# Kernel optimization log

Measured on AMD Instinct MI355X. Metric: run time of the kernel, lower is better.

## Reference

```python
import jax, jax.numpy as jnp
import numpy as np
import math

GROUPS = 16
EPS = 1e-5

def setup_inputs() -> dict:
    key = jax.random.key(0)
    ks = jax.random.split(key, 6)
    c = 256
    x = jax.random.normal(ks[0], (4, c, 64, 64), dtype=jnp.float32)
    gn_w = jnp.ones((c,), dtype=jnp.float32)
    gn_b = jnp.zeros((c,), dtype=jnp.float32)
    qkv_w = jax.random.normal(ks[1], (3 * c, c), dtype=jnp.float32) * (1.0 / math.sqrt(c))
    qkv_b = jax.random.normal(ks[2], (3 * c,), dtype=jnp.float32) * 0.02
    proj_w = jax.random.normal(ks[3], (c, c), dtype=jnp.float32) * (1.0 / math.sqrt(c))
    proj_b = jax.random.normal(ks[4], (c,), dtype=jnp.float32) * 0.02
    return {"x": x, "gn_w": gn_w, "gn_b": gn_b, "qkv_w": qkv_w,
            "qkv_b": qkv_b, "proj_w": proj_w, "proj_b": proj_b}

def group_norm(x, w, b):
    bsz, c, h, wd = x.shape
    xg = x.reshape(bsz, GROUPS, c // GROUPS, h, wd)
    mu = xg.mean(axis=(2, 3, 4), keepdims=True)
    var = xg.var(axis=(2, 3, 4), keepdims=True)
    xn = ((xg - mu) * jax.lax.rsqrt(var + EPS)).reshape(bsz, c, h, wd)
    return xn * w[None, :, None, None] + b[None, :, None, None]

def reference(x, gn_w, gn_b, qkv_w, qkv_b, proj_w, proj_b):
    b, c, h, w = x.shape
    xn = group_norm(x, gn_w, gn_b)
    # 1x1 conv == channel matmul: [b,3c,h,w]
    qkv = jnp.einsum('oc,bchw->bohw', qkv_w, xn) + qkv_b[None, :, None, None]
    q, k, v = jnp.split(qkv, 3, axis=1)          # each [b,c,h,w]
    n = h * w
    q = q.reshape(b, c, n).transpose(0, 2, 1)    # [b,n,c]
    k = k.reshape(b, c, n)                       # [b,c,n]
    v = v.reshape(b, c, n).transpose(0, 2, 1)    # [b,n,c]
    scores = jnp.einsum('bqc,bck->bqk', q, k) / jnp.sqrt(jnp.float32(c))
    attn = jax.nn.softmax(scores, axis=-1)       # [b,n,n]
    out = jnp.einsum('bqk,bkc->bqc', attn, v)    # [b,n,c]
    out = out.transpose(0, 2, 1).reshape(b, c, h, w)
    out = jnp.einsum('oc,bchw->bohw', proj_w, out) + proj_b[None, :, None, None]
    return x + out
```

## Files before the change

### kernel.cpp

```cpp
#include <hip/hip_runtime.h>


typedef unsigned short u16;
typedef unsigned char  u8;
typedef __attribute__((ext_vector_type(8)))  short short8;
typedef __attribute__((ext_vector_type(4)))  float f32x4;
typedef __attribute__((ext_vector_type(16))) float f32x16;

#define XN_OFF   0ull
#define OP_OFF   0ull
#define QW_OFF   33554432ull
#define KW_OFF   37748736ull
#define VW_OFF   41943040ull
#define LP_OFF   46137344ull
#define WQB_OFF  46399488ull
#define WPB_OFF  46792704ull

#define QSCALE 0.09016844f

__device__ __forceinline__ u16 f2bf(float x){
  unsigned u = __float_as_uint(x);
  u += 0x7fffu + ((u >> 16) & 1u);
  return (u16)(u >> 16);
}
__device__ __forceinline__ float bf2f(u16 h){
  return __uint_as_float(((unsigned)h) << 16);
}
__device__ __forceinline__ u8 f2fp8(float x){
  return (u8)(__builtin_amdgcn_cvt_pk_fp8_f32(x, x, 0, false) & 0xff);
}

__global__ __launch_bounds__(256) void gnw_k(const float* __restrict__ x, const float* __restrict__ wq,
                                             const float* __restrict__ wp, float* __restrict__ pstats,
                                             u16* __restrict__ wqb, u16* __restrict__ wpb){
  int t = threadIdx.x;
  if (blockIdx.y < 64){
    int bg = blockIdx.y, sl = blockIdx.x;
    const float* base = x + (size_t)bg*65536 + (size_t)sl*8192;
    float s = 0.f, ss = 0.f;
    for (int i = t; i < 2048; i += 256){
      float4 v = ((const float4*)base)[i];
      s  += (v.x + v.y) + (v.z + v.w);
      ss += (v.x*v.x + v.y*v.y) + (v.z*v.z + v.w*v.w);
    }
    for (int off = 32; off; off >>= 1){ s += __shfl_down(s, off, 64); ss += __shfl_down(ss, off, 64); }
    __shared__ float red[8];
    int wave = t >> 6, lane = t & 63;
    if (lane == 0){ red[wave] = s; red[4 + wave] = ss; }
    __syncthreads();
    if (t == 0){
      pstats[(bg*8 + sl)*2]     = red[0] + red[1] + red[2] + red[3];
      pstats[(bg*8 + sl)*2 + 1] = red[4] + red[5] + red[6] + red[7];
    }
  } else {
    int chunk = (blockIdx.y - 64)*8 + blockIdx.x;
    for (int it = 0; it < 16; ++it){
      int i = chunk*4096 + it*256 + t;
      int elem = i*4;
      float4 v = (elem < 196608) ? ((const float4*)wq)[i] : ((const float4*)wp)[i - 49152];
      uint2 w;
      w.x = (unsigned)f2bf(v.x) | ((unsigned)f2bf(v.y) << 16);
      w.y = (unsigned)f2bf(v.z) | ((unsigned)f2bf(v.w) << 16);
      if (elem < 196608) *(uint2*)(wqb + elem)          = w;
      else               *(uint2*)(wpb + elem - 196608) = w;
    }
  }
}

__global__ __launch_bounds__(256) void gn_apply_k(const float* __restrict__ x, const float* __restrict__ gw,
                                                  const float* __restrict__ gb, const float* __restrict__ pstats,
                                                  u16* __restrict__ xn){
  int b = blockIdx.z, c0 = blockIdx.y*64, n0 = blockIdx.x*64;
  __shared__ float tile[64*65];
  __shared__ float gmu[4], grs[4];
  int t = threadIdx.x;
  if (t < 4){
    int gidx = (b*16 + (c0 >> 4) + t)*8;
    float S = 0.f, SS = 0.f;
    for (int k2 = 0; k2 < 8; ++k2){ S += pstats[(gidx + k2)*2]; SS += pstats[(gidx + k2)*2 + 1]; }
    float mu = S*(1.f/65536.f);
    gmu[t] = mu;
    grs[t] = rsqrtf(SS*(1.f/65536.f) - mu*mu + 1e-5f);
  }
  __syncthreads();
  for (int i = 0; i < 16; ++i){
    int idx = i*256 + t;
    int cl = idx >> 6, nl = idx & 63;
    int c = c0 + cl;
    float v = x[((size_t)b*256 + c)*4096 + n0 + nl];
    tile[cl*65 + nl] = (v - gmu[cl>>4])*grs[cl>>4]*gw[c] + gb[c];
  }
  __syncthreads();
  for (int i = 0; i < 16; ++i){
    int idx = i*256 + t;
    int nl = idx >> 6, cl = idx & 63;
    xn[((size_t)b*4096 + n0 + nl)*256 + c0 + cl] = f2bf(tile[cl*65 + nl]);
  }
}

#define LDA 40
#define LDB 72
__global__ __launch_bounds__(256) void qkv_gemm_k(const u16* __restrict__ xn, const u16* __restrict__ wq,
        const float* __restrict__ qb, u8* __restrict__ q, u8* __restrict__ k, u8* __restrict__ v){
  int bx = blockIdx.x;
  int m0 = blockIdx.y*128;
  int b  = blockIdx.z;
  __shared__ u16 smem[2*128*LDB];
  u16* As = smem;
  u16* Bs = smem + 128*LDB;
  int t = threadIdx.x, lane = t & 63, wave = t >> 6;
  int wm = wave >> 1, wn = wave & 1;
  int c15 = lane & 15, g = lane >> 4;
  f32x4 acc[4][4];
  for (int mt = 0; mt < 4; ++mt) for (int nt = 0; nt < 4; ++nt) acc[mt][nt] = (f32x4){0.f,0.f,0.f,0.f};
  const u16* abase = xn + ((size_t)b*4096 + m0)*256;
  const u16* bbase = wq + (size_t)bx*128*256;
  for (int kk = 0; kk < 4; ++kk){
    int k0 = kk*64;
    for (int it = 0; it < 4; ++it){
      int idx = it*256 + t;
      int row = idx >> 3, ch = idx & 7;
      uint4 va = *(const uint4*)(abase + (size_t)row*256 + k0 + ch*8);
      *(uint4*)(As + row*LDB + ch*8) = va;
      uint4 vb = *(const uint4*)(bbase + (size_t)row*256 + k0 + ch*8);
      *(uint4*)(Bs + row*LDB + ch*8) = vb;
    }
    __syncthreads();
    for (int half = 0; half < 2; ++half){
      short8 af[4], bfr[4];
      for (int mt = 0; mt < 4; ++mt) af[mt]  = *(const short8*)(As + (wm*64 + mt*16 + c15)*LDB + half*32 + g*8);
      for (int nt = 0; nt < 4; ++nt) bfr[nt] = *(const short8*)(Bs + (wn*64 + nt*16 + c15)*LDB + half*32 + g*8);
      for (int mt = 0; mt < 4; ++mt)
        for (int nt = 0; nt < 4; ++nt)
          acc[mt][nt] = __builtin_amdgcn_mfma_f32_16x16x32_bf16(af[mt], bfr[nt], acc[mt][nt], 0, 0, 0);
    }
    __syncthreads();
  }
  if (bx < 2){
    for (int nt = 0; nt < 4; ++nt){
      int col = bx*128 + wn*64 + nt*16 + c15;
      float bias = qb[col];
      for (int mt = 0; mt < 4; ++mt){
        int m = m0 + wm*64 + mt*16 + g*4;
        for (int r = 0; r < 4; ++r)
          q[((size_t)b*4096 + m + r)*256 + col] = f2fp8(acc[mt][nt][r] + bias);
      }
    }
  } else if (bx < 4){
    for (int nt = 0; nt < 4; ++nt){
      int col = bx*128 + wn*64 + nt*16 + c15;
      int c = col - 256;
      float bias = qb[col];
      for (int mt = 0; mt < 4; ++mt){
        int m = m0 + wm*64 + mt*16 + g*4;
        for (int r = 0; r < 4; ++r){
          int n = m + r;
          size_t addr = ((size_t)b*128 + (n >> 5))*8192 +
                        (size_t)((n & 31)*256 + (((c >> 3) ^ (n & 15)) << 3) + (c & 7));
          k[addr] = f2fp8(acc[mt][nt][r] + bias);
        }
      }
    }
  } else {
    __syncthreads();
    char* Tb = (char*)smem;
    for (int nt = 0; nt < 4; ++nt){
      int o_l = wn*64 + nt*16 + c15;
      float bias = qb[bx*128 + o_l];
      for (int mt = 0; mt < 4; ++mt){
        int mb = wm*64 + mt*16 + g*4;
        unsigned p0 = (unsigned)f2bf(acc[mt][nt][0] + bias) | ((unsigned)f2bf(acc[mt][nt][1] + bias) << 16);
        unsigned p1 = (unsigned)f2bf(acc[mt][nt][2] + bias) | ((unsigned)f2bf(acc[mt][nt][3] + bias) << 16);
        int base = o_l*256 + (((mb >> 3) ^ (o_l & 7)) << 4) + ((mb & 7) << 1);
        *(unsigned*)(Tb + base)     = p0;
        *(unsigned*)(Tb + base + 4) = p1;
      }
    }
    __syncthreads();
    for (int it = 0; it < 8; ++it){
      int idx = it*256 + t;
      int ro = idx >> 4, ch = idx & 15;
      uint4 val = *(const uint4*)(Tb + ro*256 + ((ch ^ (ro & 7)) << 4));
      int c = bx*128 - 512 + ro;
      int n = m0 + ch*8;
      float f0 = bf2f((u16)(val.x & 0xffff)), f1 = bf2f((u16)(val.x >> 16));
      float f2 = bf2f((u16)(val.y & 0xffff)), f3 = bf2f((u16)(val.y >> 16));
      float f4 = bf2f((u16)(val.z & 0xffff)), f5 = bf2f((u16)(val.z >> 16));
      float f6 = bf2f((u16)(val.w & 0xffff)), f7 = bf2f((u16)(val.w >> 16));
      int w0 = __builtin_amdgcn_cvt_pk_fp8_f32(f0, f1, 0, false);
      w0     = __builtin_amdgcn_cvt_pk_fp8_f32(f2, f3, w0, true);
      int w1 = __builtin_amdgcn_cvt_pk_fp8_f32(f4, f5, 0, false);
      w1     = __builtin_amdgcn_cvt_pk_fp8_f32(f6, f7, w1, true);
      size_t addr = ((size_t)b*128 + (n >> 5))*8192 +
                    (size_t)(c*32 + ((((n >> 3) & 3) ^ ((c >> 2) & 3)) << 3));
      uint2 wv; wv.x = (unsigned)w0; wv.y = (unsigned)w1;
      *(uint2*)(v + addr) = wv;
    }
  }
}

__global__ __launch_bounds__(256, 2) void flash_k(const u8* __restrict__ q, const u8* __restrict__ kt,
                                                  const u8* __restrict__ vt, u16* __restrict__ opart,
                                                  float* __restrict__ lpart){
  int n0 = blockIdx.x*128;
  int jh = blockIdx.y;
  int b  = blockIdx.z;
  __shared__ char buf[2][16384];
  int t = threadIdx.x, lane = t & 63, wave = t >> 6;
  int il = lane & 31;
  int h  = lane >> 5;

  uint2 qf[16];
  const u8* qrow = q + ((size_t)b*4096 + n0 + wave*32 + il)*256;
  #pragma unroll
  for (int s = 0; s < 16; ++s) qf[s] = *(const uint2*)(qrow + s*16 + h*8);

  f32x16 oacc[8];
  #pragma unroll
  for (int ct = 0; ct < 8; ++ct){
    #pragma unroll
    for (int r = 0; r < 16; ++r) oacc[ct][r] = 0.f;
  }
  float lsum = 0.f;

  size_t tb0 = ((size_t)b*128 + jh*32) * 8192;
  const char* gK = (const char*)kt + tb0;
  const char* gV = (const char*)vt + tb0;
  const char* gsrc = (wave < 2) ? (gK + wave*4096) : (gV + (wave - 2)*4096);
  unsigned lds_off = wave*4096;

  {
    const char* g0 = gsrc + (size_t)lane*16;
    #pragma unroll
    for (int i = 0; i < 4; ++i)
      __builtin_amdgcn_global_load_lds((const __attribute__((address_space(1))) void*)(g0 + i*1024),
          (__attribute__((address_space(3))) void*)((char*)buf[0] + lds_off + i*1024), 16, 0, 0);
    const char* g1 = gsrc + 8192 + (size_t)lane*16;
    #pragma unroll
    for (int i = 0; i < 4; ++i)
      __builtin_amdgcn_global_load_lds((const __attribute__((address_space(1))) void*)(g1 + i*1024),
          (__attribute__((address_space(3))) void*)((char*)buf[1] + lds_off + i*1024), 16, 0, 0);
  }

  for (int jt = 0; jt < 32; ++jt){
    int p = jt & 1;
    asm volatile("" ::: "memory");
    if (jt < 31) __builtin_amdgcn_s_waitcnt(0x0F74);
    else         __builtin_amdgcn_s_waitcnt(0x0F70);
    __builtin_amdgcn_s_barrier();
    asm volatile("" ::: "memory");

    const char* klds = buf[p];
    const char* vlds = buf[p] + 8192;

    f32x16 s0, s1;
    #pragma unroll
    for (int r = 0; r < 16; ++r){ s0[r] = 0.f; s1[r] = 0.f; }
    #pragma unroll
    for (int s = 0; s < 16; s += 2){
      long kf0 = *(const long*)(klds + il*256 + (((2*s + h)       ^ (il & 15)) << 3));
      long kf1 = *(const long*)(klds + il*256 + (((2*(s+1) + h)   ^ (il & 15)) << 3));
      s0 = __builtin_amdgcn_mfma_f32_32x32x16_fp8_fp8(kf0, *(const long*)&qf[s],   s0, 0, 0, 0);
      s1 = __builtin_amdgcn_mfma_f32_32x32x16_fp8_fp8(kf1, *(const long*)&qf[s+1], s1, 0, 0, 0);
    }
    float pv[16];
    #pragma unroll
    for (int r = 0; r < 16; ++r){
      float e = exp2f((s0[r] + s1[r]) * QSCALE);
      pv[r] = e;
      lsum += e;
    }
    long pa[2];
    #pragma unroll
    for (int s2 = 0; s2 < 2; ++s2){
      int q0 = __builtin_amdgcn_cvt_pk_fp8_f32(pv[8*s2+0], pv[8*s2+1], 0, false);
      q0     = __builtin_amdgcn_cvt_pk_fp8_f32(pv[8*s2+2], pv[8*s2+3], q0, true);
      int q1 = __builtin_amdgcn_cvt_pk_fp8_f32(pv[8*s2+4], pv[8*s2+5], 0, false);
      q1     = __builtin_amdgcn_cvt_pk_fp8_f32(pv[8*s2+6], pv[8*s2+7], q1, true);
      int e  = h ? q0 : q1;
      int rr = __shfl_xor(e, 32, 64);
      unsigned lo = (unsigned)(h ? rr : q0);
      unsigned hi = (unsigned)(h ? q1 : rr);
      pa[s2] = ((long)hi << 32) | (long)lo;
    }
    #pragma unroll
    for (int s2 = 0; s2 < 2; ++s2){
      #pragma unroll
      for (int ct = 0; ct < 8; ++ct){
        int c = ct*32 + il;
        long vf = *(const long*)(vlds + c*32 + (((2*s2 + h) ^ ((c >> 2) & 3)) << 3));
        oacc[ct] = __builtin_amdgcn_mfma_f32_32x32x16_fp8_fp8(pa[s2], vf, oacc[ct], 0, 0, 0);
      }
    }

    asm volatile("" ::: "memory");
    __builtin_amdgcn_s_waitcnt(0xC07F);
    __builtin_amdgcn_s_barrier();
    asm volatile("" ::: "memory");
    if (jt + 2 < 32){
      const char* gn2 = gsrc + (size_t)(jt + 2)*8192 + (size_t)lane*16;
      #pragma unroll
      for (int i = 0; i < 4; ++i)
        __builtin_amdgcn_global_load_lds((const __attribute__((address_space(1))) void*)(gn2 + i*1024),
            (__attribute__((address_space(3))) void*)((char*)buf[p] + lds_off + i*1024), 16, 0, 0);
    }
  }

  float tot = lsum + __shfl_xor(lsum, 32, 64);
  if (h == 0) lpart[(size_t)(jh*4 + b)*4096 + n0 + wave*32 + il] = tot;
  u16* obase = opart + ((size_t)(jh*4 + b)*4096 + n0 + wave*32)*256;
  #pragma unroll
  for (int ct = 0; ct < 8; ++ct){
    #pragma unroll
    for (int r = 0; r < 16; ++r){
      int i = (r & 3) + 8*(r >> 2) + 4*h;
      obase[(size_t)i*256 + ct*32 + il] = f2bf(oacc[ct][r]);
    }
  }
}

__global__ __launch_bounds__(256) void proj_gemm_k(const u16* __restrict__ opart, const float* __restrict__ lpart,
        const u16* __restrict__ wp, const float* __restrict__ pb, const float* __restrict__ x,
        float* __restrict__ out){
  int n0 = blockIdx.x*64;
  int b  = blockIdx.y;
  __shared__ u16 As[256*LDA];
  __shared__ u16 Bs[64*LDA];
  __shared__ float linv[64];
  int t = threadIdx.x, lane = t & 63, wave = t >> 6;
  int c15 = lane & 15, g = lane >> 4;
  if (t < 64){
    size_t row = (size_t)b*4096 + n0 + t;
    linv[t] = 1.0f / (lpart[row] + lpart[16384 + row] + lpart[32768 + row] + lpart[49152 + row]);
  }
  f32x4 acc[4][4];
  for (int mt = 0; mt < 4; ++mt) for (int nt = 0; nt < 4; ++nt) acc[mt][nt] = (f32x4){0.f,0.f,0.f,0.f};
  __syncthreads();
  for (int kk = 0; kk < 8; ++kk){
    int k0 = kk*32;
    for (int it = 0; it < 4; ++it){
      int idx = it*256 + t;
      int row = idx >> 2, ch = idx & 3;
      *(uint4*)(As + row*LDA + ch*8) = *(const uint4*)(wp + (size_t)row*256 + k0 + ch*8);
    }
    {
      int row = t >> 2, ch = t & 3;
      const u16* bptr = opart + ((size_t)b*4096 + n0 + row)*256 + k0 + ch*8;
      uint4 o0 = *(const uint4*)(bptr);
      uint4 o1 = *(const uint4*)(bptr + 4194304ull);
      uint4 o2 = *(const uint4*)(bptr + 8388608ull);
      uint4 o3 = *(const uint4*)(bptr + 12582912ull);
      float inv = linv[row];
      const unsigned* u0 = (const unsigned*)&o0;
      const unsigned* u1 = (const unsigned*)&o1;
      const unsigned* u2 = (const unsigned*)&o2;
      const unsigned* u3 = (const unsigned*)&o3;
      uint4 w;
      unsigned* wpk = (unsigned*)&w;
      for (int i = 0; i < 4; ++i){
        float lo = (bf2f((u16)(u0[i] & 0xffff)) + bf2f((u16)(u1[i] & 0xffff)) +
                    bf2f((u16)(u2[i] & 0xffff)) + bf2f((u16)(u3[i] & 0xffff))) * inv;
        float hi = (bf2f((u16)(u0[i] >> 16))    + bf2f((u16)(u1[i] >> 16)) +
                    bf2f((u16)(u2[i] >> 16))    + bf2f((u16)(u3[i] >> 16)))    * inv;
        wpk[i] = (unsigned)f2bf(lo) | ((unsigned)f2bf(hi) << 16);
      }
      *(uint4*)(Bs + row*LDA + ch*8) = w;
    }
    __syncthreads();
    short8 af[4], bfr[4];
    for (int mt = 0; mt < 4; ++mt) af[mt]  = *(const short8*)(As + (wave*64 + mt*16 + c15)*LDA + g*8);
    for (int nt = 0; nt < 4; ++nt) bfr[nt] = *(const short8*)(Bs + (nt*16 + c15)*LDA + g*8);
    for (int mt = 0; mt < 4; ++mt)
      for (int nt = 0; nt < 4; ++nt)
        acc[mt][nt] = __builtin_amdgcn_mfma_f32_16x16x32_bf16(af[mt], bfr[nt], acc[mt][nt], 0, 0, 0);
    __syncthreads();
  }
  for (int mt = 0; mt < 4; ++mt){
    for (int r = 0; r < 4; ++r){
      int o = wave*64 + mt*16 + g*4 + r;
      float bias = pb[o];
      for (int nt = 0; nt < 4; ++nt){
        int n = n0 + nt*16 + c15;
        size_t off = ((size_t)b*256 + o)*4096 + n;
        out[off] = x[off] + bias + acc[mt][nt][r];
      }
    }
  }
}

extern "C" void kernel_launch(void* const* d_in, const int* in_sizes, int n_in,
                              void* d_out, int out_size, void* d_ws, size_t ws_size,
                              hipStream_t stream){
  (void)in_sizes; (void)n_in; (void)out_size; (void)ws_size;
  const float* x     = (const float*)d_in[0];
  const float* gw    = (const float*)d_in[1];
  const float* gb    = (const float*)d_in[2];
  const float* qkvw  = (const float*)d_in[3];
  const float* qkvb  = (const float*)d_in[4];
  const float* projw = (const float*)d_in[5];
  const float* projb = (const float*)d_in[6];
  float* out = (float*)d_out;
  char* ws = (char*)d_ws;

  u16*   xn    = (u16*)(ws + XN_OFF);
  u16*   op    = (u16*)(ws + OP_OFF);
  u8*    qws   = (u8*)(ws + QW_OFF);
  float* pstat = (float*)(ws + QW_OFF);
  u8*    kws   = (u8*)(ws + KW_OFF);
  u8*    vws   = (u8*)(ws + VW_OFF);
  float* lp    = (float*)(ws + LP_OFF);
  u16*   wqb   = (u16*)(ws + WQB_OFF);
  u16*   wpb   = (u16*)(ws + WPB_OFF);

  gnw_k<<<dim3(8, 66), 256, 0, stream>>>(x, qkvw, projw, pstat, wqb, wpb);
  gn_apply_k<<<dim3(64, 4, 4), 256, 0, stream>>>(x, gw, gb, pstat, xn);
  qkv_gemm_k<<<dim3(6, 32, 4), 256, 0, stream>>>(xn, wqb, qkvb, qws, kws, vws);
  flash_k<<<dim3(32, 4, 4), 256, 0, stream>>>(qws, kws, vws, op, lp);
  proj_gemm_k<<<dim3(64, 4), 256, 0, stream>>>(op, lp, wpb, projb, x, out);
}
```

Measured before the change: 174.5 us.

## Vectorize Q/K fp8 epilogue via swapped MFMA operands; widen proj GEMM to 512 threads

For the Q and K column blocks of the QKV GEMM, the MFMA operand order is swapped so each lane holds four consecutive channels. The epilogue can then pack four fp8 values with two cvt_pk_fp8 calls and write one 32-bit store, instead of four scattered byte stores with per-element swizzle math. The projection GEMM moves to 512 threads with a 2x2 wave split, a 64-wide K step and half as many K iterations. This gives more waves per block and fewer barriers, at the cost of more LDS per block and fewer accumulators per wave.

After: 179.0 us. 2.6% more time.

```diff
diff --git a/kernel.cpp b/kernel.cpp
--- a/kernel.cpp
+++ b/kernel.cpp
@@ -25,9 +25,6 @@
 }
 __device__ __forceinline__ float bf2f(u16 h){
   return __uint_as_float(((unsigned)h) << 16);
-}
-__device__ __forceinline__ u8 f2fp8(float x){
-  return (u8)(__builtin_amdgcn_cvt_pk_fp8_f32(x, x, 0, false) & 0xff);
 }
 
 __global__ __launch_bounds__(256) void gnw_k(const float* __restrict__ x, const float* __restrict__ wq,
@@ -98,7 +95,6 @@
   }
 }
 
-#define LDA 40
 #define LDB 72
 __global__ __launch_bounds__(256) void qkv_gemm_k(const u16* __restrict__ xn, const u16* __restrict__ wq,
         const float* __restrict__ qb, u8* __restrict__ q, u8* __restrict__ k, u8* __restrict__ v){
@@ -112,7 +108,7 @@
   int wm = wave >> 1, wn = wave & 1;
   int c15 = lane & 15, g = lane >> 4;
   f32x4 acc[4][4];
-  for (int mt = 0; mt < 4; ++mt) for (int nt = 0; nt < 4; ++nt) acc[mt][nt] = (f32x4){0.f,0.f,0.f,0.f};
+  for (int i = 0; i < 4; ++i) for (int j = 0; j < 4; ++j) acc[i][j] = (f32x4){0.f,0.f,0.f,0.f};
   const u16* abase = xn + ((size_t)b*4096 + m0)*256;
   const u16* bbase = wq + (size_t)bx*128*256;
   for (int kk = 0; kk < 4; ++kk){
@@ -128,37 +124,44 @@
     __syncthreads();
     for (int half = 0; half < 2; ++half){
       short8 af[4], bfr[4];
-      for (int mt = 0; mt < 4; ++mt) af[mt]  = *(const short8*)(As + (wm*64 + mt*16 + c15)*LDB + half*32 + g*8);
-      for (int nt = 0; nt < 4; ++nt) bfr[nt] = *(const short8*)(Bs + (wn*64 + nt*16 + c15)*LDB + half*32 + g*8);
-      for (int mt = 0; mt < 4; ++mt)
-        for (int nt = 0; nt < 4; ++nt)
-          acc[mt][nt] = __builtin_amdgcn_mfma_f32_16x16x32_bf16(af[mt], bfr[nt], acc[mt][nt], 0, 0, 0);
+      for (int pt = 0; pt < 4; ++pt) af[pt]  = *(const short8*)(As + (wm*64 + pt*16 + c15)*LDB + half*32 + g*8);
+      for (int ot = 0; ot < 4; ++ot) bfr[ot] = *(const short8*)(Bs + (wn*64 + ot*16 + c15)*LDB + half*32 + g*8);
+      if (bx < 4){
+        for (int ot = 0; ot < 4; ++ot)
+          for (int pt = 0; pt < 4; ++pt)
+            acc[ot][pt] = __builtin_amdgcn_mfma_f32_16x16x32_bf16(bfr[ot], af[pt], acc[ot][pt], 0, 0, 0);
+      } else {
+        for (int mt = 0; mt < 4; ++mt)
+          for (int nt = 0; nt < 4; ++nt)
+            acc[mt][nt] = __builtin_amdgcn_mfma_f32_16x16x32_bf16(af[mt], bfr[nt], acc[mt][nt], 0, 0, 0);
+      }
     }
     __syncthreads();
   }
   if (bx < 2){
-    for (int nt = 0; nt < 4; ++nt){
-      int col = bx*128 + wn*64 + nt*16 + c15;
-      float bias = qb[col];
-      for (int mt = 0; mt < 4; ++mt){
-        int m = m0 + wm*64 + mt*16 + g*4;
-        for (int r = 0; r < 4; ++r)
-          q[((size_t)b*4096 + m + r)*256 + col] = f2fp8(acc[mt][nt][r] + bias);
+    for (int ot = 0; ot < 4; ++ot){
+      int col = bx*128 + wn*64 + ot*16 + g*4;
+      float4 b4 = *(const float4*)(qb + col);
+      for (int pt = 0; pt < 4; ++pt){
+        int n = m0 + wm*64 + pt*16 + c15;
+        f32x4 a = acc[ot][pt];
+        int w0 = __builtin_amdgcn_cvt_pk_fp8_f32(a[0] + b4.x, a[1] + b4.y, 0, false);
+        w0     = __builtin_amdgcn_cvt_pk_fp8_f32(a[2] + b4.z, a[3] + b4.w, w0, true);
+        *(unsigned*)(q + ((size_t)b*4096 + n)*256 + col) = (unsigned)w0;
       }
     }
   } else if (bx < 4){
-    for (int nt = 0; nt < 4; ++nt){
-      int col = bx*128 + wn*64 + nt*16 + c15;
-      int c = col - 256;
-      float bias = qb[col];
-      for (int mt = 0; mt < 4; ++mt){
-        int m = m0 + wm*64 + mt*16 + g*4;
-        for (int r = 0; r < 4; ++r){
-          int n = m + r;
-          size_t addr = ((size_t)b*128 + (n >> 5))*8192 +
-                        (size_t)((n & 31)*256 + (((c >> 3) ^ (n & 15)) << 3) + (c & 7));
-          k[addr] = f2fp8(acc[mt][nt][r] + bias);
-        }
+    for (int ot = 0; ot < 4; ++ot){
+      int cb = (bx - 2)*128 + wn*64 + ot*16 + g*4;
+      float4 b4 = *(const float4*)(qb + 256 + cb);
+      for (int pt = 0; pt < 4; ++pt){
+        int n = m0 + wm*64 + pt*16 + c15;
+        f32x4 a = acc[ot][pt];
+        int w0 = __builtin_amdgcn_cvt_pk_fp8_f32(a[0] + b4.x, a[1] + b4.y, 0, false);
+        w0     = __builtin_amdgcn_cvt_pk_fp8_f32(a[2] + b4.z, a[3] + b4.w, w0, true);
+        size_t addr = ((size_t)b*128 + (n >> 5))*8192 +
+                      (size_t)((n & 31)*256 + (((cb >> 3) ^ (n & 15)) << 3) + (cb & 7));
+        *(unsigned*)(k + addr) = (unsigned)w0;
       }
     }
   } else {
@@ -319,32 +322,33 @@
   }
 }
 
-__global__ __launch_bounds__(256) void proj_gemm_k(const u16* __restrict__ opart, const float* __restrict__ lpart,
+__global__ __launch_bounds__(512) void proj_gemm_k(const u16* __restrict__ opart, const float* __restrict__ lpart,
         const u16* __restrict__ wp, const float* __restrict__ pb, const float* __restrict__ x,
         float* __restrict__ out){
   int n0 = blockIdx.x*64;
   int b  = blockIdx.y;
-  __shared__ u16 As[256*LDA];
-  __shared__ u16 Bs[64*LDA];
+  __shared__ u16 As[256*LDB];
+  __shared__ u16 Bs[64*LDB];
   __shared__ float linv[64];
   int t = threadIdx.x, lane = t & 63, wave = t >> 6;
+  int ow = wave >> 1, nw = wave & 1;
   int c15 = lane & 15, g = lane >> 4;
   if (t < 64){
     size_t row = (size_t)b*4096 + n0 + t;
     linv[t] = 1.0f / (lpart[row] + lpart[16384 + row] + lpart[32768 + row] + lpart[49152 + row]);
   }
-  f32x4 acc[4][4];
-  for (int mt = 0; mt < 4; ++mt) for (int nt = 0; nt < 4; ++nt) acc[mt][nt] = (f32x4){0.f,0.f,0.f,0.f};
+  f32x4 acc[4][2];
+  for (int mt = 0; mt < 4; ++mt) for (int nt = 0; nt < 2; ++nt) acc[mt][nt] = (f32x4){0.f,0.f,0.f,0.f};
   __syncthreads();
-  for (int kk = 0; kk < 8; ++kk){
-    int k0 = kk*32;
+  for (int kk = 0; kk < 4; ++kk){
+    int k0 = kk*64;
     for (int it = 0; it < 4; ++it){
-      int idx = it*256 + t;
-      int row = idx >> 2, ch = idx & 3;
-      *(uint4*)(As + row*LDA + ch*8) = *(const uint4*)(wp + (size_t)row*256 + k0 + ch*8);
+      int idx = it*512 + t;
+      int row = idx >> 3, ch = idx & 7;
+      *(uint4*)(As + row*LDB + ch*8) = *(const uint4*)(wp + (size_t)row*256 + k0 + ch*8);
     }
     {
-      int row = t >> 2, ch = t & 3;
+      int row = t >> 3, ch = t & 7;
       const u16* bptr = opart + ((size_t)b*4096 + n0 + row)*256 + k0 + ch*8;
       uint4 o0 = *(const uint4*)(bptr);
       uint4 o1 = *(const uint4*)(bptr + 4194304ull);
@@ -364,23 +368,25 @@
                     bf2f((u16)(u2[i] >> 16))    + bf2f((u16)(u3[i] >> 16)))    * inv;
         wpk[i] = (unsigned)f2bf(lo) | ((unsigned)f2bf(hi) << 16);
       }
-      *(uint4*)(Bs + row*LDA + ch*8) = w;
-    }
-    __syncthreads();
-    short8 af[4], bfr[4];
-    for (int mt = 0; mt < 4; ++mt) af[mt]  = *(const short8*)(As + (wave*64 + mt*16 + c15)*LDA + g*8);
-    for (int nt = 0; nt < 4; ++nt) bfr[nt] = *(const short8*)(Bs + (nt*16 + c15)*LDA + g*8);
-    for (int mt = 0; mt < 4; ++mt)
-      for (int nt = 0; nt < 4; ++nt)
-        acc[mt][nt] = __builtin_amdgcn_mfma_f32_16x16x32_bf16(af[mt], bfr[nt], acc[mt][nt], 0, 0, 0);
+      *(uint4*)(Bs + row*LDB + ch*8) = w;
+    }
+    __syncthreads();
+    for (int half = 0; half < 2; ++half){
+      short8 af[4], bfr[2];
+      for (int mt = 0; mt < 4; ++mt) af[mt]  = *(const short8*)(As + (ow*64 + mt*16 + c15)*LDB + half*32 + g*8);
+      for (int nt = 0; nt < 2; ++nt) bfr[nt] = *(const short8*)(Bs + (nw*32 + nt*16 + c15)*LDB + half*32 + g*8);
+      for (int mt = 0; mt < 4; ++mt)
+        for (int nt = 0; nt < 2; ++nt)
+          acc[mt][nt] = __builtin_amdgcn_mfma_f32_16x16x32_bf16(af[mt], bfr[nt], acc[mt][nt], 0, 0, 0);
+    }
     __syncthreads();
   }
   for (int mt = 0; mt < 4; ++mt){
     for (int r = 0; r < 4; ++r){
-      int o = wave*64 + mt*16 + g*4 + r;
+      int o = ow*64 + mt*16 + g*4 + r;
       float bias = pb[o];
-      for (int nt = 0; nt < 4; ++nt){
-        int n = n0 + nt*16 + c15;
+      for (int nt = 0; nt < 2; ++nt){
+        int n = n0 + nw*32 + nt*16 + c15;
         size_t off = ((size_t)b*256 + o)*4096 + n;
         out[off] = x[off] + bias + acc[mt][nt][r];
       }
@@ -416,5 +422,5 @@
   gn_apply_k<<<dim3(64, 4, 4), 256, 0, stream>>>(x, gw, gb, pstat, xn);
   qkv_gemm_k<<<dim3(6, 32, 4), 256, 0, stream>>>(xn, wqb, qkvb, qws, kws, vws);
   flash_k<<<dim3(32, 4, 4), 256, 0, stream>>>(qws, kws, vws, op, lp);
-  proj_gemm_k<<<dim3(64, 4), 256, 0, stream>>>(op, lp, wpb, projb, x, out);
-}
+  proj_gemm_k<<<dim3(64, 4), 512, 0, stream>>>(op, lp, wpb, projb, x, out);
+}
```

## Fuse group-norm apply into QKV GEMM A-tile load and use raw v_exp_f32

Applied to the files above, without the earlier changes.

Drops the separate gn_apply kernel and the bf16 xn buffer. The QKV GEMM now reads fp32 x directly, normalizes with per-group stats and affine weights held in LDS, and writes the transposed bf16 A tile into shared memory. The pstats buffer moves to its own workspace offset so it no longer aliases the Q buffer, which the GEMM now writes while still reading the stats. Each of the 6 column blocks re-reads and re-normalizes x, trading a kernel launch and a global round trip for redundant loads and transpose stores into LDS that may bank-conflict. The flash kernel's exp2f is also replaced with the raw v_exp_f32 instruction, skipping denormal and range handling.

Result: no change. 177.5 us (+1.7%).

```diff
diff --git a/kernel.cpp b/kernel.cpp
--- a/kernel.cpp
+++ b/kernel.cpp
@@ -7,7 +7,6 @@
 typedef __attribute__((ext_vector_type(4)))  float f32x4;
 typedef __attribute__((ext_vector_type(16))) float f32x16;
 
-#define XN_OFF   0ull
 #define OP_OFF   0ull
 #define QW_OFF   33554432ull
 #define KW_OFF   37748736ull
@@ -15,8 +14,11 @@
 #define LP_OFF   46137344ull
 #define WQB_OFF  46399488ull
 #define WPB_OFF  46792704ull
+#define ST_OFF   46923776ull
 
 #define QSCALE 0.09016844f
+#define LDA 40
+#define LDB 72
 
 __device__ __forceinline__ u16 f2bf(float x){
   unsigned u = __float_as_uint(x);
@@ -28,6 +30,11 @@
 }
 __device__ __forceinline__ u8 f2fp8(float x){
   return (u8)(__builtin_amdgcn_cvt_pk_fp8_f32(x, x, 0, false) & 0xff);
+}
+__device__ __forceinline__ float fast_exp2(float x){
+  float r;
+  asm("v_exp_f32 %0, %1" : "=v"(r) : "v"(x));
+  return r;
 }
 
 __global__ __launch_bounds__(256) void gnw_k(const float* __restrict__ x, const float* __restrict__ wq,
@@ -67,63 +74,69 @@
   }
 }
 
-__global__ __launch_bounds__(256) void gn_apply_k(const float* __restrict__ x, const float* __restrict__ gw,
-                                                  const float* __restrict__ gb, const float* __restrict__ pstats,
-                                                  u16* __restrict__ xn){
-  int b = blockIdx.z, c0 = blockIdx.y*64, n0 = blockIdx.x*64;
-  __shared__ float tile[64*65];
-  __shared__ float gmu[4], grs[4];
-  int t = threadIdx.x;
-  if (t < 4){
-    int gidx = (b*16 + (c0 >> 4) + t)*8;
+__global__ __launch_bounds__(256) void qkv_gemm_k(const float* __restrict__ x, const float* __restrict__ gw,
+        const float* __restrict__ gb, const float* __restrict__ pstats, const u16* __restrict__ wq,
+        const float* __restrict__ qb, u8* __restrict__ q, u8* __restrict__ k, u8* __restrict__ v){
+  int bx = blockIdx.x;
+  int m0 = blockIdx.y*128;
+  int b  = blockIdx.z;
+  __shared__ u16 smem[2*128*LDB];
+  __shared__ float gwl[256], gbl[256], gmu[16], grs[16];
+  u16* As = smem;
+  u16* Bs = smem + 128*LDB;
+  int t = threadIdx.x, lane = t & 63, wave = t >> 6;
+  int wm = wave >> 1, wn = wave & 1;
+  int c15 = lane & 15, g = lane >> 4;
+
+  if (t < 16){
+    int gidx = (b*16 + t)*8;
     float S = 0.f, SS = 0.f;
     for (int k2 = 0; k2 < 8; ++k2){ S += pstats[(gidx + k2)*2]; SS += pstats[(gidx + k2)*2 + 1]; }
     float mu = S*(1.f/65536.f);
     gmu[t] = mu;
     grs[t] = rsqrtf(SS*(1.f/65536.f) - mu*mu + 1e-5f);
   }
+  gwl[t] = gw[t];
+  gbl[t] = gb[t];
   __syncthreads();
-  for (int i = 0; i < 16; ++i){
-    int idx = i*256 + t;
-    int cl = idx >> 6, nl = idx & 63;
-    int c = c0 + cl;
-    float v = x[((size_t)b*256 + c)*4096 + n0 + nl];
-    tile[cl*65 + nl] = (v - gmu[cl>>4])*grs[cl>>4]*gw[c] + gb[c];
-  }
-  __syncthreads();
-  for (int i = 0; i < 16; ++i){
-    int idx = i*256 + t;
-    int nl = idx >> 6, cl = idx & 63;
-    xn[((size_t)b*4096 + n0 + nl)*256 + c0 + cl] = f2bf(tile[cl*65 + nl]);
-  }
-}
-
-#define LDA 40
-#define LDB 72
-__global__ __launch_bounds__(256) void qkv_gemm_k(const u16* __restrict__ xn, const u16* __restrict__ wq,
-        const float* __restrict__ qb, u8* __restrict__ q, u8* __restrict__ k, u8* __restrict__ v){
-  int bx = blockIdx.x;
-  int m0 = blockIdx.y*128;
-  int b  = blockIdx.z;
-  __shared__ u16 smem[2*128*LDB];
-  u16* As = smem;
-  u16* Bs = smem + 128*LDB;
-  int t = threadIdx.x, lane = t & 63, wave = t >> 6;
-  int wm = wave >> 1, wn = wave & 1;
-  int c15 = lane & 15, g = lane >> 4;
+
   f32x4 acc[4][4];
   for (int mt = 0; mt < 4; ++mt) for (int nt = 0; nt < 4; ++nt) acc[mt][nt] = (f32x4){0.f,0.f,0.f,0.f};
-  const u16* abase = xn + ((size_t)b*4096 + m0)*256;
+  const float* xb = x + (size_t)b*256*4096 + m0;
   const u16* bbase = wq + (size_t)bx*128*256;
+
   for (int kk = 0; kk < 4; ++kk){
     int k0 = kk*64;
     for (int it = 0; it < 4; ++it){
       int idx = it*256 + t;
       int row = idx >> 3, ch = idx & 7;
-      uint4 va = *(const uint4*)(abase + (size_t)row*256 + k0 + ch*8);
-      *(uint4*)(As + row*LDB + ch*8) = va;
-      uint4 vb = *(const uint4*)(bbase + (size_t)row*256 + k0 + ch*8);
-      *(uint4*)(Bs + row*LDB + ch*8) = vb;
+      *(uint4*)(Bs + row*LDB + ch*8) = *(const uint4*)(bbase + (size_t)row*256 + k0 + ch*8);
+    }
+    for (int it = 0; it < 2; ++it){
+      int idx = it*256 + t;
+      int cq = idx >> 5, nq = idx & 31;
+      int c0 = k0 + cq*4, nb = nq*4;
+      const float* xr = xb + (size_t)c0*4096 + nb;
+      float4 xv0 = *(const float4*)(xr);
+      float4 xv1 = *(const float4*)(xr + 4096);
+      float4 xv2 = *(const float4*)(xr + 8192);
+      float4 xv3 = *(const float4*)(xr + 12288);
+      int grp = c0 >> 4;
+      float mu = gmu[grp], rs = grs[grp];
+      float a0 = rs*gwl[c0+0], b0 = gbl[c0+0] - mu*a0;
+      float a1 = rs*gwl[c0+1], b1 = gbl[c0+1] - mu*a1;
+      float a2 = rs*gwl[c0+2], b2 = gbl[c0+2] - mu*a2;
+      float a3 = rs*gwl[c0+3], b3 = gbl[c0+3] - mu*a3;
+      const float* f0 = (const float*)&xv0;
+      const float* f1 = (const float*)&xv1;
+      const float* f2 = (const float*)&xv2;
+      const float* f3 = (const float*)&xv3;
+      for (int j = 0; j < 4; ++j){
+        uint2 w;
+        w.x = (unsigned)f2bf(f0[j]*a0 + b0) | ((unsigned)f2bf(f1[j]*a1 + b1) << 16);
+        w.y = (unsigned)f2bf(f2[j]*a2 + b2) | ((unsigned)f2bf(f3[j]*a3 + b3) << 16);
+        *(uint2*)(As + (nb + j)*LDB + cq*4) = w;
+      }
     }
     __syncthreads();
     for (int half = 0; half < 2; ++half){
@@ -266,7 +279,7 @@
     float pv[16];
     #pragma unroll
     for (int r = 0; r < 16; ++r){
-      float e = exp2f((s0[r] + s1[r]) * QSCALE);
+      float e = fast_exp2((s0[r] + s1[r]) * QSCALE);
       pv[r] = e;
       lsum += e;
     }
@@ -402,19 +415,17 @@
   float* out = (float*)d_out;
   char* ws = (char*)d_ws;
 
-  u16*   xn    = (u16*)(ws + XN_OFF);
   u16*   op    = (u16*)(ws + OP_OFF);
   u8*    qws   = (u8*)(ws + QW_OFF);
-  float* pstat = (float*)(ws + QW_OFF);
   u8*    kws   = (u8*)(ws + KW_OFF);
   u8*    vws   = (u8*)(ws + VW_OFF);
   float* lp    = (float*)(ws + LP_OFF);
   u16*   wqb   = (u16*)(ws + WQB_OFF);
   u16*   wpb   = (u16*)(ws + WPB_OFF);
+  float* pstat = (float*)(ws + ST_OFF);
 
   gnw_k<<<dim3(8, 66), 256, 0, stream>>>(x, qkvw, projw, pstat, wqb, wpb);
-  gn_apply_k<<<dim3(64, 4, 4), 256, 0, stream>>>(x, gw, gb, pstat, xn);
-  qkv_gemm_k<<<dim3(6, 32, 4), 256, 0, stream>>>(xn, wqb, qkvb, qws, kws, vws);
+  qkv_gemm_k<<<dim3(6, 32, 4), 256, 0, stream>>>(x, gw, gb, pstat, wqb, qkvb, qws, kws, vws);
   flash_k<<<dim3(32, 4, 4), 256, 0, stream>>>(qws, kws, vws, op, lp);
   proj_gemm_k<<<dim3(64, 4), 256, 0, stream>>>(op, lp, wpb, projb, x, out);
 }
```
